# Kernel tuning notes

Hardware: AMD Instinct MI355X
Metric: run time of the kernel (lower is better)

The kernel has to match this reference:

```python
import jax, jax.numpy as jnp
import numpy as np

B, A, N, D = 512, 3, 64, 32


def _lte(x):
    """LTETransform: straight-through hard threshold (forward: 1[x>0], backward: identity)."""
    hard = (x > 0).astype(x.dtype)
    return x + jax.lax.stop_gradient(hard - x)


def setup_inputs() -> dict:
    key = jax.random.key(0)
    k1, k2 = jax.random.split(key)
    feature = jax.random.normal(k1, (B, N, D), dtype=jnp.float32)
    indicator = jax.random.normal(k2, (A, N, D), dtype=jnp.float32)
    return {"feature": feature, "indicator": indicator}


def reference(feature, indicator):
    # gate = LTE(DotWeight(indicator[0], indicator[1])) -> [N, N]
    gate = _lte(jnp.einsum('id,jd->ij', indicator[0], indicator[1]))

    # QKV[a,i,j,:,:] = indicator[a,i,:] (outer) indicator[a,j,:]  (rank-1), so
    # input[b,a,i,j,d] = (feature[b,i,:] . indicator[a,i,:]) * indicator[a,j,d]
    s = jnp.einsum('bnd,and->ban', feature, indicator)  # [B, 3, N]

    # query[b,i,j,d] = elu(s[b,0,i] * ind[0,j,d]) + 1              [B,N,N,D]
    q = jax.nn.elu(s[:, 0, :, None, None] * indicator[0][None, None, :, :]) + 1.0
    # key.transpose(1,2)[b,i,j,d] = elu(s[b,1,j] * ind[1,i,d]) + 1  [B,N,N,D]
    k_t = jax.nn.elu(s[:, 1, None, :, None] * indicator[1][None, :, None, :]) + 1.0

    score = jnp.einsum('bijd,bijd->bij', q, k_t)  # [B, N, N]
    probs = jax.nn.softmax(score, axis=-1)
    score_hat = probs * gate[None, :, :]

    # value[b,i,j,d] = s[b,2,i] * ind[2,j,d];  out = sum_j scoreHat * value
    out = s[:, 2, :, None] * jnp.einsum('bij,jd->bid', score_hat, indicator[2])
    return out  # [B, N, D]
```

## Files before the change

kernel.cpp:

```cpp
#include <hip/hip_runtime.h>

namespace {
constexpr int Bsz = 512;
constexpr int N   = 64;
constexpr int D   = 32;
constexpr int PD  = 36;

__global__ void gate_kernel(const float* __restrict__ ind, float* __restrict__ gate) {
    int i = blockIdx.x;
    int j = threadIdx.x;
    const float* u = ind + 0 * N * D + i * D;
    const float* v = ind + 1 * N * D + j * D;
    float acc = 0.f;
#pragma unroll
    for (int d = 0; d < D; ++d) acc += u[d] * v[d];
    gate[i * N + j] = (acc > 0.f) ? 1.f : 0.f;
}

__device__ __forceinline__ float elup1(float x) {
    return __expf(fminf(x, 0.f)) + fmaxf(x, 0.f);
}

__global__ __launch_bounds__(512, 4) void fused_kernel(
        const float* __restrict__ feature,
        const float* __restrict__ ind,
        const float* __restrict__ gate,
        float* __restrict__ out) {
    __shared__ float ind_lds[3][N][PD];
    __shared__ float feat_lds[N][PD];
    __shared__ float s_lds[3][N];

    const int b    = blockIdx.x;
    const int t    = threadIdx.x;
    const int lane = t & 63;
    const int wave = t >> 6;

    {
        const float4* src = reinterpret_cast<const float4*>(ind);
#pragma unroll
        for (int f4 = t; f4 < 3 * N * D / 4; f4 += 512) {
            int a = f4 / (N * D / 4);
            int r = f4 % (N * D / 4);
            int n = r / (D / 4);
            int k = r % (D / 4);
            *reinterpret_cast<float4*>(&ind_lds[a][n][k * 4]) = src[f4];
        }
        const float4* fsrc = reinterpret_cast<const float4*>(feature + (size_t)b * N * D);
        if (t < N * D / 4) {
            int n = t / (D / 4);
            int k = t % (D / 4);
            *reinterpret_cast<float4*>(&feat_lds[n][k * 4]) = fsrc[t];
        }
    }
    __syncthreads();

    if (t < 3 * N) {
        int a = t >> 6, n = t & 63;
        float acc = 0.f;
#pragma unroll
        for (int d = 0; d < D; ++d) acc += feat_lds[n][d] * ind_lds[a][n][d];
        s_lds[a][n] = acc;
    }
    __syncthreads();

    const int   j   = lane;
    const float s1j = s_lds[1][j];

#pragma unroll 1
    for (int r = 0; r < 8; ++r) {
        const int   i   = wave * 8 + r;
        const float s0i = s_lds[0][i];

        float score = 0.f;
#pragma unroll
        for (int k = 0; k < D / 4; ++k) {
            float4 u4 = *reinterpret_cast<const float4*>(&ind_lds[0][j][k * 4]);
            float4 v4 = *reinterpret_cast<const float4*>(&ind_lds[1][i][k * 4]);
            float uu[4] = {u4.x, u4.y, u4.z, u4.w};
            float vv[4] = {v4.x, v4.y, v4.z, v4.w};
#pragma unroll
            for (int c = 0; c < 4; ++c) {
                float q  = elup1(s0i * uu[c]);
                float kt = elup1(s1j * vv[c]);
                score += q * kt;
            }
        }

        float m = score;
#pragma unroll
        for (int off = 32; off >= 1; off >>= 1) m = fmaxf(m, __shfl_xor(m, off));
        float e = __expf(score - m);
        float ssum = e;
#pragma unroll
        for (int off = 32; off >= 1; off >>= 1) ssum += __shfl_xor(ssum, off);

        float sh = (e / ssum) * gate[i * N + j];

        const int d    = lane & 31;
        const int half = lane >> 5;
        float acc = 0.f;
#pragma unroll
        for (int jj = 0; jj < 32; ++jj) {
            int   jidx = half * 32 + jj;
            float shv  = __shfl(sh, jidx);
            acc += shv * ind_lds[2][jidx][d];
        }
        acc += __shfl_xor(acc, 32);
        if (half == 0) {
            out[((size_t)b * N + i) * D + d] = s_lds[2][i] * acc;
        }
    }
}
}

extern "C" void kernel_launch(void* const* d_in, const int* in_sizes, int n_in,
                              void* d_out, int out_size, void* d_ws, size_t ws_size,
                              hipStream_t stream) {
    const float* feature = (const float*)d_in[0];
    const float* ind     = (const float*)d_in[1];
    float*       gate    = (float*)d_ws;
    float*       out     = (float*)d_out;

    gate_kernel<<<N, N, 0, stream>>>(ind, gate);
    fused_kernel<<<Bsz, 512, 0, stream>>>(feature, ind, gate, out);
}
```

Baseline: 93.74 us.

## Fuse gate into main kernel, split rows across two blocks, restructure output matmul

Removes the separate gate kernel launch by computing the gate rows in shared memory inside the fused kernel. Each batch is split across two blocks of 32 rows, which doubles the grid and raises the launch-bounds occupancy hint. Exponentials are rewritten with exp2 and rcp intrinsics, and the query-side indicator values are held in registers. The final weighted sum now goes through a shared-memory buffer with float4 loads and stores instead of per-element shuffles. In exchange, the indicator tensor is loaded and the gate is recomputed in every block, adding redundant work.

```diff
diff --git a/kernel.cpp b/kernel.cpp
--- a/kernel.cpp
+++ b/kernel.cpp
@@ -1,113 +1,154 @@
 #include <hip/hip_runtime.h>
 
 namespace {
-constexpr int Bsz = 512;
-constexpr int N   = 64;
-constexpr int D   = 32;
-constexpr int PD  = 36;
+constexpr int N  = 64;
+constexpr int D  = 32;
+constexpr int PD = 36;
+constexpr int SHP = 68;
+constexpr float LOG2E = 1.4426950408889634f;
+constexpr float LN2   = 0.6931471805599453f;
 
-__global__ void gate_kernel(const float* __restrict__ ind, float* __restrict__ gate) {
-    int i = blockIdx.x;
-    int j = threadIdx.x;
-    const float* u = ind + 0 * N * D + i * D;
-    const float* v = ind + 1 * N * D + j * D;
-    float acc = 0.f;
-#pragma unroll
-    for (int d = 0; d < D; ++d) acc += u[d] * v[d];
-    gate[i * N + j] = (acc > 0.f) ? 1.f : 0.f;
+#if __has_builtin(__builtin_amdgcn_exp2f)
+__device__ __forceinline__ float fexp2(float x) { return __builtin_amdgcn_exp2f(x); }
+#else
+__device__ __forceinline__ float fexp2(float x) { return exp2f(x); }
+#endif
+#if __has_builtin(__builtin_amdgcn_rcpf)
+__device__ __forceinline__ float frcp(float x) { return __builtin_amdgcn_rcpf(x); }
+#else
+__device__ __forceinline__ float frcp(float x) { return 1.0f / x; }
+#endif
+
+__device__ __forceinline__ float elup1_scaled(float xL) {
+    return fmaf(fmaxf(xL, 0.f), LN2, fexp2(fminf(xL, 0.f)));
 }
 
-__device__ __forceinline__ float elup1(float x) {
-    return __expf(fminf(x, 0.f)) + fmaxf(x, 0.f);
-}
-
-__global__ __launch_bounds__(512, 4) void fused_kernel(
+__global__ __launch_bounds__(512, 6) void fused(
         const float* __restrict__ feature,
         const float* __restrict__ ind,
-        const float* __restrict__ gate,
         float* __restrict__ out) {
     __shared__ float ind_lds[3][N][PD];
-    __shared__ float feat_lds[N][PD];
     __shared__ float s_lds[3][N];
+    __shared__ float gate_lds[32][N];
+    __shared__ float sh_lds[32][SHP];
 
-    const int b    = blockIdx.x;
     const int t    = threadIdx.x;
     const int lane = t & 63;
     const int wave = t >> 6;
+    const int blk  = blockIdx.x;
+    const int b    = blk >> 1;
+    const int i_base = (blk & 1) * 32;
 
     {
         const float4* src = reinterpret_cast<const float4*>(ind);
 #pragma unroll
-        for (int f4 = t; f4 < 3 * N * D / 4; f4 += 512) {
-            int a = f4 / (N * D / 4);
-            int r = f4 % (N * D / 4);
-            int n = r / (D / 4);
-            int k = r % (D / 4);
-            *reinterpret_cast<float4*>(&ind_lds[a][n][k * 4]) = src[f4];
-        }
-        const float4* fsrc = reinterpret_cast<const float4*>(feature + (size_t)b * N * D);
-        if (t < N * D / 4) {
-            int n = t / (D / 4);
-            int k = t % (D / 4);
-            *reinterpret_cast<float4*>(&feat_lds[n][k * 4]) = fsrc[t];
+        for (int idx = t; idx < 3 * N * D / 4; idx += 512) {
+            int a = idx >> 9;
+            int r = idx & 511;
+            int n = r >> 3;
+            int k = r & 7;
+            *reinterpret_cast<float4*>(&ind_lds[a][n][k * 4]) = src[idx];
         }
     }
     __syncthreads();
 
-    if (t < 3 * N) {
-        int a = t >> 6, n = t & 63;
-        float acc = 0.f;
+    {
+        const int i_loc = t >> 4;
+        const int jq    = t & 15;
+        float4 acc = {0.f, 0.f, 0.f, 0.f};
 #pragma unroll
-        for (int d = 0; d < D; ++d) acc += feat_lds[n][d] * ind_lds[a][n][d];
-        s_lds[a][n] = acc;
+        for (int dq = 0; dq < 8; ++dq) {
+            float4 a4 = *reinterpret_cast<const float4*>(&ind_lds[0][i_base + i_loc][dq * 4]);
+#pragma unroll
+            for (int c = 0; c < 4; ++c) {
+                float4 b4 = *reinterpret_cast<const float4*>(&ind_lds[1][jq + 16 * c][dq * 4]);
+                (&acc.x)[c] += a4.x * b4.x + a4.y * b4.y + a4.z * b4.z + a4.w * b4.w;
+            }
+        }
+#pragma unroll
+        for (int c = 0; c < 4; ++c)
+            gate_lds[i_loc][jq + 16 * c] = ((&acc.x)[c] > 0.f) ? 1.f : 0.f;
+
+        if (t < 3 * N) {
+            int a = t >> 6, n = t & 63;
+            const float4* frow = reinterpret_cast<const float4*>(feature + ((size_t)b * N + n) * D);
+            float sa = 0.f;
+#pragma unroll
+            for (int k = 0; k < 8; ++k) {
+                float4 f4 = frow[k];
+                float4 i4 = *reinterpret_cast<const float4*>(&ind_lds[a][n][k * 4]);
+                sa += f4.x * i4.x + f4.y * i4.y + f4.z * i4.z + f4.w * i4.w;
+            }
+            s_lds[a][n] = sa;
+        }
     }
     __syncthreads();
 
-    const int   j   = lane;
-    const float s1j = s_lds[1][j];
+    float4 u[8];
+#pragma unroll
+    for (int k = 0; k < 8; ++k)
+        u[k] = *reinterpret_cast<const float4*>(&ind_lds[0][lane][k * 4]);
+    const float s1jL = s_lds[1][lane] * LOG2E;
 
 #pragma unroll 1
-    for (int r = 0; r < 8; ++r) {
-        const int   i   = wave * 8 + r;
-        const float s0i = s_lds[0][i];
+    for (int r = 0; r < 4; ++r) {
+        const int   i_loc = wave * 4 + r;
+        const int   ig    = i_base + i_loc;
+        const float s0iL  = s_lds[0][ig] * LOG2E;
+        const float s2i   = s_lds[2][ig];
 
         float score = 0.f;
 #pragma unroll
-        for (int k = 0; k < D / 4; ++k) {
-            float4 u4 = *reinterpret_cast<const float4*>(&ind_lds[0][j][k * 4]);
-            float4 v4 = *reinterpret_cast<const float4*>(&ind_lds[1][i][k * 4]);
-            float uu[4] = {u4.x, u4.y, u4.z, u4.w};
-            float vv[4] = {v4.x, v4.y, v4.z, v4.w};
+        for (int k = 0; k < 8; ++k) {
+            float4 v4 = *reinterpret_cast<const float4*>(&ind_lds[1][ig][k * 4]);
 #pragma unroll
             for (int c = 0; c < 4; ++c) {
-                float q  = elup1(s0i * uu[c]);
-                float kt = elup1(s1j * vv[c]);
-                score += q * kt;
+                float q  = elup1_scaled(s0iL * (&u[k].x)[c]);
+                float kt = elup1_scaled(s1jL * (&v4.x)[c]);
+                score = fmaf(q, kt, score);
             }
         }
 
         float m = score;
 #pragma unroll
         for (int off = 32; off >= 1; off >>= 1) m = fmaxf(m, __shfl_xor(m, off));
-        float e = __expf(score - m);
+        float e = fexp2((score - m) * LOG2E);
         float ssum = e;
 #pragma unroll
         for (int off = 32; off >= 1; off >>= 1) ssum += __shfl_xor(ssum, off);
 
-        float sh = (e / ssum) * gate[i * N + j];
+        float g   = gate_lds[i_loc][lane];
+        float shv = (e * g) * (frcp(ssum) * s2i);
+        sh_lds[i_loc][lane] = shv;
+    }
+    __syncthreads();
 
-        const int d    = lane & 31;
-        const int half = lane >> 5;
-        float acc = 0.f;
+    {
+        const int i_loc = t >> 4;
+        const int sub   = t & 15;
+        const int dq    = sub & 7;
+        const int jh    = sub >> 3;
+        float4 acc = {0.f, 0.f, 0.f, 0.f};
 #pragma unroll
-        for (int jj = 0; jj < 32; ++jj) {
-            int   jidx = half * 32 + jj;
-            float shv  = __shfl(sh, jidx);
-            acc += shv * ind_lds[2][jidx][d];
+        for (int jj = 0; jj < 32; jj += 4) {
+            int j = jh * 32 + jj;
+            float4 sh4 = *reinterpret_cast<const float4*>(&sh_lds[i_loc][j]);
+#pragma unroll
+            for (int c = 0; c < 4; ++c) {
+                float4 v4 = *reinterpret_cast<const float4*>(&ind_lds[2][j + c][dq * 4]);
+                float  w  = (&sh4.x)[c];
+                acc.x = fmaf(w, v4.x, acc.x);
+                acc.y = fmaf(w, v4.y, acc.y);
+                acc.z = fmaf(w, v4.z, acc.z);
+                acc.w = fmaf(w, v4.w, acc.w);
+            }
         }
-        acc += __shfl_xor(acc, 32);
-        if (half == 0) {
-            out[((size_t)b * N + i) * D + d] = s_lds[2][i] * acc;
+        acc.x += __shfl_xor(acc.x, 8);
+        acc.y += __shfl_xor(acc.y, 8);
+        acc.z += __shfl_xor(acc.z, 8);
+        acc.w += __shfl_xor(acc.w, 8);
+        if (jh == 0) {
+            *reinterpret_cast<float4*>(out + ((size_t)b * N + i_base + i_loc) * D + dq * 4) = acc;
         }
     }
 }
@@ -118,9 +159,6 @@
                               hipStream_t stream) {
     const float* feature = (const float*)d_in[0];
     const float* ind     = (const float*)d_in[1];
-    float*       gate    = (float*)d_ws;
     float*       out     = (float*)d_out;
-
-    gate_kernel<<<N, N, 0, stream>>>(ind, gate);
-    fused_kernel<<<Bsz, 512, 0, stream>>>(feature, ind, gate, out);
+    fused<<<1024, 512, 0, stream>>>(feature, ind, out);
 }
```

Measured after the change: 88.81 us. -5.3%, faster.
